# Optimization experiments

Hardware: AMD Instinct MI355X
Metric: run time of the kernel (lower is better)

## Reference

```python
import jax, jax.numpy as jnp
import numpy as np

PC_RANGE = (-50.0, -50.0, -4.0, 50.0, 50.0, 4.0)
IMG_H, IMG_W = 256.0, 704.0
EPS = 1e-5


def _bilinear_sample(feat, u, v):
    # feat [H,W,C]; u,v [M] in [0,1]; matches F.grid_sample(align_corners=False, padding_mode='zeros')
    H, W, _ = feat.shape
    x = u * W - 0.5
    y = v * H - 0.5
    x0 = jnp.floor(x)
    y0 = jnp.floor(y)
    dx = (x - x0)[:, None]
    dy = (y - y0)[:, None]
    x0 = x0.astype(jnp.int32)
    y0 = y0.astype(jnp.int32)

    def g(xi, yi):
        inb = ((xi >= 0) & (xi < W) & (yi >= 0) & (yi < H)).astype(feat.dtype)[:, None]
        return feat[jnp.clip(yi, 0, H - 1), jnp.clip(xi, 0, W - 1)] * inb

    return (g(x0, y0) * (1 - dx) * (1 - dy) + g(x0 + 1, y0) * dx * (1 - dy)
            + g(x0, y0 + 1) * (1 - dx) * dy + g(x0 + 1, y0 + 1) * dx * dy)


def _conv1x1(t, w, b):
    return jnp.einsum('bchw,oc->bohw', t, w) + b[None, :, None, None]


def _inorm(t, eps=1e-5):
    # InstanceNorm2d (affine=False): normalize per (b, c) over spatial dims
    m = t.mean(axis=(2, 3), keepdims=True)
    var = t.var(axis=(2, 3), keepdims=True)
    return (t - m) * jax.lax.rsqrt(var + eps)


def _forward(feat, lidar2img, bev_pos, pe_w1, pe_b1, pe_w2, pe_b2, pe_w3, pe_b3,
             c1_w, c1_b, c2_w, c2_b, c3_w, c3_b):
    B, N, C, Hf, Wf = feat.shape
    _, P, Hb, Wb, _ = bev_pos.shape
    Q = Hb * Wb
    lo = jnp.asarray(PC_RANGE[:3], feat.dtype)
    hi = jnp.asarray(PC_RANGE[3:], feat.dtype)
    # 'b p h w d -> b (h w) p d', then scale normalized coords into pc_range
    ref01 = jnp.transpose(bev_pos, (0, 2, 3, 1, 4)).reshape(B, Q, P, 3)
    ref = ref01 * (hi - lo) + lo
    # project through per-camera lidar2img (homogeneous)
    pts = jnp.concatenate([ref, jnp.ones_like(ref[..., :1])], axis=-1)  # [B,Q,P,4]
    cam = jnp.einsum('bnij,bqpj->bnqpi', lidar2img, pts)                # [B,N,Q,P,4]
    homo = cam[..., 2]
    z = jnp.maximum(homo, EPS)
    u = cam[..., 0] / z / IMG_W
    v = cam[..., 1] / z / IMG_H
    valid = ((homo > EPS) & (u > 0.0) & (u < 1.0) & (v > 0.0) & (v < 1.0)).astype(feat.dtype)
    # bilinear gather per camera; feats to channel-last ('b n (g c) h w -> (b g) n h w c', G=1)
    fmap = jnp.transpose(feat, (0, 1, 3, 4, 2)).reshape(B * N, Hf, Wf, C)
    samp = jax.vmap(_bilinear_sample)(fmap, u.reshape(B * N, Q * P), v.reshape(B * N, Q * P))
    samp = samp.reshape(B, N, Q, P, C) * valid[..., None]
    samp = samp.sum(axis=1)  # sum over cameras -> [B,Q,P,C]
    # PositionalEncodingMap(3 -> 256 -> 256 -> 128) on normalized reference points
    pe = jax.nn.relu(ref01 @ pe_w1 + pe_b1)
    pe = jax.nn.relu(pe @ pe_w2 + pe_b2)
    pe = pe @ pe_w3 + pe_b3
    samp = samp + pe
    # 'b (h w) g p c -> b (p g c) h w' with g=1
    x = jnp.transpose(samp.reshape(B, Hb, Wb, P, C), (0, 3, 4, 1, 2)).reshape(B, P * C, Hb, Wb)
    gelu = lambda t: jax.nn.gelu(t, approximate=False)
    x = gelu(_inorm(_conv1x1(x, c1_w, c1_b)))
    x = gelu(_inorm(_conv1x1(x, c2_w, c2_b)))
    x = _conv1x1(x, c3_w, c3_b)
    return x


def setup_inputs() -> dict:
    key = jax.random.key(0)
    ks = jax.random.split(key, 16)
    B, N, C, Hf, Wf = 1, 6, 128, 32, 88
    P, Hb, Wb = 4, 160, 160
    E = 128
    MID = 256
    s = 0.02
    return {
        'feat': jax.random.normal(ks[0], (B, N, C, Hf, Wf), jnp.float32),
        'lidar2img': jax.random.normal(ks[1], (B, N, 4, 4), jnp.float32),
        'bev_pos': jax.random.uniform(ks[2], (B, P, Hb, Wb, 3), jnp.float32),
        'pe_w1': jax.random.normal(ks[3], (3, MID), jnp.float32) * s,
        'pe_b1': jnp.zeros((MID,), jnp.float32),
        'pe_w2': jax.random.normal(ks[4], (MID, MID), jnp.float32) * s,
        'pe_b2': jnp.zeros((MID,), jnp.float32),
        'pe_w3': jax.random.normal(ks[5], (MID, E), jnp.float32) * s,
        'pe_b3': jnp.zeros((E,), jnp.float32),
        'c1_w': jax.random.normal(ks[6], (4 * E, P * 128), jnp.float32) * s,
        'c1_b': jnp.zeros((4 * E,), jnp.float32),
        'c2_w': jax.random.normal(ks[7], (E, 4 * E), jnp.float32) * s,
        'c2_b': jnp.zeros((E,), jnp.float32),
        'c3_w': jax.random.normal(ks[8], (E, E), jnp.float32) * s,
        'c3_b': jnp.zeros((E,), jnp.float32),
    }


def reference(feat, lidar2img, bev_pos, pe_w1, pe_b1, pe_w2, pe_b2, pe_w3, pe_b3,
              c1_w, c1_b, c2_w, c2_b, c3_w, c3_b):
    return _forward(feat, lidar2img, bev_pos, pe_w1, pe_b1, pe_w2, pe_b2, pe_w3, pe_b3,
                    c1_w, c1_b, c2_w, c2_b, c3_w, c3_b)
```

## Files before the change

kernel.cpp:

```cpp
#include <hip/hip_runtime.h>
#include <cstdint>
#include <cstddef>

using frag8 = __attribute__((ext_vector_type(8))) short;
using f32x4 = __attribute__((ext_vector_type(4))) float;

__device__ __forceinline__ float b2f_bits(unsigned short u) {
    union { uint32_t u32; float f; } x; x.u32 = ((uint32_t)u) << 16; return x.f;
}
__device__ __forceinline__ float b2f_lo(uint32_t pk) {
    return __builtin_bit_cast(float, pk << 16);
}
__device__ __forceinline__ float b2f_hi(uint32_t pk) {
    return __builtin_bit_cast(float, pk & 0xffff0000u);
}
__device__ __forceinline__ unsigned short f2b(float f) {
    uint32_t u = __builtin_bit_cast(uint32_t, f);
    uint32_t r = (u + 0x7fffu + ((u >> 16) & 1u)) >> 16;
    return (unsigned short)r;
}
__device__ __forceinline__ uint32_t cvtpk_bf16(float lo, float hi) {
    uint32_t r;
    asm("v_cvt_pk_bf16_f32 %0, %1, %2" : "=v"(r) : "v"(lo), "v"(hi));
    return r;
}

#define HF 32
#define WFEAT 88
#define NCAM 6
#define NPT 102400
#define BM 128
#define BN 128
#define BK 64

__global__ __launch_bounds__(256) void k_prep(const float* __restrict__ feat,
                                              const float* __restrict__ pw2,
                                              const float* __restrict__ pw3,
                                              const float* __restrict__ c1w,
                                              const float* __restrict__ c2w,
                                              const float* __restrict__ c3w,
                                              unsigned short* __restrict__ featT,
                                              unsigned short* __restrict__ W2Tb,
                                              unsigned short* __restrict__ W3Tb,
                                              unsigned short* __restrict__ C1Wb,
                                              unsigned short* __restrict__ C2Wb,
                                              unsigned short* __restrict__ C3Wb,
                                              float* __restrict__ stats) {
    __shared__ unsigned short tile[64 * 132];
    int b = blockIdx.x, t = threadIdx.x;
    if (b < 264) {
        int n = b / 44;
        int s0 = (b - n * 44) * 64;
        #pragma unroll
        for (int i = 0; i < 32; ++i) {
            int e = i * 256 + t;
            int c = e >> 6, sl = e & 63;
            tile[sl * 132 + c] = f2b(feat[(size_t)(n * 128 + c) * 2816 + s0 + sl]);
        }
        __syncthreads();
        #pragma unroll
        for (int j = 0; j < 8; ++j) {
            int flat = j * 1024 + t * 4;
            int sl = flat >> 7, c = flat & 127;
            ushort4 v = *(const ushort4*)(tile + sl * 132 + c);
            *(ushort4*)(featT + (size_t)(n * 2816 + s0 + sl) * 128 + c) = v;
        }
        return;
    }
    b -= 264;
    if (b < 256) {
        int idx = b * 256 + t;
        int r = idx >> 8, c = idx & 255;
        W2Tb[c * 256 + r] = f2b(pw2[idx]);
        return;
    }
    b -= 256;
    if (b < 128) {
        int idx = b * 256 + t;
        int r = idx >> 7, c = idx & 127;
        W3Tb[c * 256 + r] = f2b(pw3[idx]);
        return;
    }
    b -= 128;
    if (b < 1024) { int idx = b * 256 + t; C1Wb[idx] = f2b(c1w[idx]); return; }
    b -= 1024;
    if (b < 256)  { int idx = b * 256 + t; C2Wb[idx] = f2b(c2w[idx]); return; }
    b -= 256;
    if (b < 64)   { int idx = b * 256 + t; C3Wb[idx] = f2b(c3w[idx]); return; }
    #pragma unroll
    for (int j = 0; j < 10; ++j) stats[t * 10 + j] = 0.f;
}

__global__ __launch_bounds__(256) void k_sample2(const unsigned short* __restrict__ featT,
                                                 const float* __restrict__ l2i,
                                                 const float* __restrict__ bev,
                                                 unsigned short* __restrict__ samp) {
    int pt = blockIdx.x * 4 + (threadIdx.x >> 6);
    int lane = threadIdx.x & 63;
    int c2 = lane * 2;
    int q = pt >> 2, p = pt & 3;
    int h = q / 160, w = q - h * 160;
    const float* bv = bev + ((p * 160 + h) * 160 + w) * 3;
    float rx = bv[0] * 100.f - 50.f;
    float ry = bv[1] * 100.f - 50.f;
    float rz = bv[2] * 8.f - 4.f;
    float acc0 = 0.f, acc1 = 0.f;
    #pragma unroll
    for (int n = 0; n < NCAM; ++n) {
        const float* M = l2i + n * 16;
        float c0   = M[0] * rx + M[1] * ry + M[2]  * rz + M[3];
        float c1v  = M[4] * rx + M[5] * ry + M[6]  * rz + M[7];
        float homo = M[8] * rx + M[9] * ry + M[10] * rz + M[11];
        float z = fmaxf(homo, 1e-5f);
        float u = c0 / z / 704.0f;
        float v = c1v / z / 256.0f;
        if (homo > 1e-5f && u > 0.f && u < 1.f && v > 0.f && v < 1.f) {
            float fx = u * (float)WFEAT - 0.5f;
            float fy = v * (float)HF - 0.5f;
            float fx0 = floorf(fx), fy0 = floorf(fy);
            float dx = fx - fx0, dy = fy - fy0;
            int x0 = (int)fx0, y0 = (int)fy0;
            float wxa = (x0 < 0) ? dx : 1.f - dx;
            float wxb = (x0 >= 0 && x0 < WFEAT - 1) ? dx : 0.f;
            float wya = (y0 < 0) ? dy : 1.f - dy;
            float wyb = (y0 >= 0 && y0 < HF - 1) ? dy : 0.f;
            int bx = max(x0, 0), by = max(y0, 0);
            const unsigned short* base = featT + (((n * HF + by) * WFEAT + bx) << 7) + c2;
            uint32_t p00 = *(const uint32_t*)(base);
            uint32_t p01 = *(const uint32_t*)(base + 128);
            uint32_t p10 = *(const uint32_t*)(base + WFEAT * 128);
            uint32_t p11 = *(const uint32_t*)(base + WFEAT * 128 + 128);
            float w00 = wxa * wya, w01 = wxb * wya, w10 = wxa * wyb, w11 = wxb * wyb;
            acc0 += w00 * b2f_lo(p00) + w01 * b2f_lo(p01) + w10 * b2f_lo(p10) + w11 * b2f_lo(p11);
            acc1 += w00 * b2f_hi(p00) + w01 * b2f_hi(p01) + w10 * b2f_hi(p10) + w11 * b2f_hi(p11);
        }
    }
    uint32_t outpk = (uint32_t)f2b(acc0) | ((uint32_t)f2b(acc1) << 16);
    *(uint32_t*)(samp + (size_t)pt * 128 + c2) = outpk;
}

__device__ __forceinline__ void stage_tile(const unsigned short* __restrict__ g, int ld,
                                           unsigned short* lds, int wave, int lane) {
    #pragma unroll
    for (int j = 0; j < 4; ++j) {
        int idx = wave * 256 + j * 64 + lane;
        int r = idx >> 3;
        int cs = idx & 7;
        int cl = cs ^ (r & 7);
        __builtin_amdgcn_global_load_lds(
            (const __attribute__((address_space(1))) void*)(g + (size_t)r * ld + cl * 8),
            (__attribute__((address_space(3))) void*)(lds + wave * 2048 + j * 512),
            16, 0, 0);
    }
}

__device__ __forceinline__ frag8 frag_read(const unsigned short* lds, int row, int chunk) {
    return *(const frag8*)(lds + row * 64 + ((chunk ^ (row & 7)) << 3));
}

__device__ __forceinline__ void mma_tile(const unsigned short* As, const unsigned short* Bs,
                                         int wm, int wn, int lane, f32x4 (&acc)[4][4]) {
    int lm = lane & 15, lq = lane >> 4;
    #pragma unroll
    for (int kk = 0; kk < 2; ++kk) {
        frag8 a[4], b[4];
        #pragma unroll
        for (int t = 0; t < 4; ++t) a[t] = frag_read(As, wm * 64 + t * 16 + lm, kk * 4 + lq);
        #pragma unroll
        for (int t = 0; t < 4; ++t) b[t] = frag_read(Bs, wn * 64 + t * 16 + lm, kk * 4 + lq);
        #pragma unroll
        for (int tm = 0; tm < 4; ++tm)
            #pragma unroll
            for (int tn = 0; tn < 4; ++tn)
                acc[tm][tn] = __builtin_amdgcn_mfma_f32_16x16x32_bf16(a[tm], b[tn], acc[tm][tn], 0, 0, 0);
    }
}

template <int KT>
__device__ __forceinline__ void gemm_loop_pipe(const unsigned short* __restrict__ A, int ldA,
                                               const unsigned short* __restrict__ B, int ldB,
                                               unsigned short (*As)[BM * BK],
                                               unsigned short (*Bs)[BN * BK],
                                               int wave, int lane, int wm, int wn,
                                               f32x4 (&acc)[4][4]) {
    stage_tile(A, ldA, As[0], wave, lane);
    stage_tile(B, ldB, Bs[0], wave, lane);
    if (KT > 1) {
        stage_tile(A + BK, ldA, As[1], wave, lane);
        stage_tile(B + BK, ldB, Bs[1], wave, lane);
    }
    #pragma unroll
    for (int kt = 0; kt < KT; ++kt) {
        int cur = kt & 1;
        if (kt + 1 < KT) asm volatile("s_waitcnt vmcnt(8)" ::: "memory");
        else             asm volatile("s_waitcnt vmcnt(0)" ::: "memory");
        __builtin_amdgcn_s_barrier();
        mma_tile(As[cur], Bs[cur], wm, wn, lane, acc);
        asm volatile("s_waitcnt lgkmcnt(0)" ::: "memory");
        __builtin_amdgcn_s_barrier();
        if (kt + 2 < KT) {
            stage_tile(A + (kt + 2) * BK, ldA, As[cur], wave, lane);
            stage_tile(B + (kt + 2) * BK, ldB, Bs[cur], wave, lane);
        }
    }
}

__device__ __forceinline__ void build_h1_2(const float* __restrict__ wls, float x, float y, float z,
                                           int r, int c0, int kt, unsigned short* __restrict__ As) {
    #pragma unroll
    for (int j = 0; j < 2; ++j) {
        int cl = c0 + j;
        const float* wp = wls + kt * 64 + cl * 8;
        float4 a0l = *(const float4*)(wp),       a0h = *(const float4*)(wp + 4);
        float4 a1l = *(const float4*)(wp + 256), a1h = *(const float4*)(wp + 260);
        float4 a2l = *(const float4*)(wp + 512), a2h = *(const float4*)(wp + 516);
        float4 bbl = *(const float4*)(wp + 768), bbh = *(const float4*)(wp + 772);
        float v0 = fmaxf(x * a0l.x + y * a1l.x + z * a2l.x + bbl.x, 0.f);
        float v1 = fmaxf(x * a0l.y + y * a1l.y + z * a2l.y + bbl.y, 0.f);
        float v2 = fmaxf(x * a0l.z + y * a1l.z + z * a2l.z + bbl.z, 0.f);
        float v3 = fmaxf(x * a0l.w + y * a1l.w + z * a2l.w + bbl.w, 0.f);
        float v4 = fmaxf(x * a0h.x + y * a1h.x + z * a2h.x + bbh.x, 0.f);
        float v5 = fmaxf(x * a0h.y + y * a1h.y + z * a2h.y + bbh.y, 0.f);
        float v6 = fmaxf(x * a0h.z + y * a1h.z + z * a2h.z + bbh.z, 0.f);
        float v7 = fmaxf(x * a0h.w + y * a1h.w + z * a2h.w + bbh.w, 0.f);
        uint32_t q0 = cvtpk_bf16(v0, v1), q1 = cvtpk_bf16(v2, v3);
        uint32_t q2 = cvtpk_bf16(v4, v5), q3 = cvtpk_bf16(v6, v7);
        *(uint4*)(As + r * 64 + ((cl ^ (r & 7)) << 3)) = make_uint4(q0, q1, q2, q3);
    }
}

__global__ __launch_bounds__(256) void k_pe123(const float* __restrict__ bev,
                                               const float* __restrict__ pw1,
                                               const float* __restrict__ pb1,
                                               const unsigned short* __restrict__ W2t,
                                               const float* __restrict__ pb2,
                                               const unsigned short* __restrict__ W3t,
                                               const float* __restrict__ pb3,
                                               const unsigned short* __restrict__ samp,
                                               unsigned short* __restrict__ X) {
    __shared__ __align__(16) char smem[78592];
    unsigned short* As  = (unsigned short*)smem;
    unsigned short* Bs0 = (unsigned short*)(smem + 8192);
    unsigned short* Bs1 = (unsigned short*)(smem + 40960);
    float* wls  = (float*)(smem + 73728);
    float* bevs = (float*)(smem + 77824);
    int t = threadIdx.x, lane = t & 63, wave = t >> 6;
    int m0 = blockIdx.x * 64;
    {
        int i = t * 4;
        int j = i >> 8, c = i & 255;
        float4 v = (j < 3) ? *(const float4*)(pw1 + j * 256 + c)
                           : *(const float4*)(pb1 + c);
        *(float4*)(wls + i) = v;
    }
    if (t < 64) {
        int m = m0 + t;
        int q = m >> 2, p = m & 3;
        int h = q / 160, w = q - h * 160;
        const float* bv = bev + ((size_t)((p * 160 + h) * 160 + w)) * 3;
        bevs[t] = bv[0]; bevs[64 + t] = bv[1]; bevs[128 + t] = bv[2];
    }
    __syncthreads();
    int r = t & 63;
    int c0 = (t >> 6) * 2;
    float x = bevs[r], y = bevs[64 + r], z = bevs[128 + r];
    int lm = lane & 15, lq = lane >> 4;
    f32x4 acc[4][4] = {};
    stage_tile(W2t, 256, Bs0, wave, lane);
    stage_tile(W2t + 128 * 256, 256, Bs0 + 8192, wave, lane);
    stage_tile(W2t + BK, 256, Bs1, wave, lane);
    stage_tile(W2t + 128 * 256 + BK, 256, Bs1 + 8192, wave, lane);
    #pragma unroll
    for (int kt = 0; kt < 4; ++kt) {
        unsigned short* Bcur = (kt & 1) ? Bs1 : Bs0;
        build_h1_2(wls, x, y, z, r, c0, kt, As);
        asm volatile("s_waitcnt lgkmcnt(0)" ::: "memory");
        if (kt + 1 < 4) asm volatile("s_waitcnt vmcnt(8)" ::: "memory");
        else            asm volatile("s_waitcnt vmcnt(0)" ::: "memory");
        __builtin_amdgcn_s_barrier();
        #pragma unroll
        for (int kk = 0; kk < 2; ++kk) {
            int ch = kk * 4 + lq;
            frag8 a[4], b[4];
            #pragma unroll
            for (int tt = 0; tt < 4; ++tt) a[tt] = frag_read(As, tt * 16 + lm, ch);
            #pragma unroll
            for (int tn = 0; tn < 4; ++tn) b[tn] = frag_read(Bcur, wave * 64 + tn * 16 + lm, ch);
            #pragma unroll
            for (int tm = 0; tm < 4; ++tm)
                #pragma unroll
                for (int tn = 0; tn < 4; ++tn)
                    acc[tm][tn] = __builtin_amdgcn_mfma_f32_16x16x32_bf16(a[tm], b[tn], acc[tm][tn], 0, 0, 0);
        }
        asm volatile("s_waitcnt lgkmcnt(0)" ::: "memory");
        __builtin_amdgcn_s_barrier();
        if (kt + 2 < 4) {
            stage_tile(W2t + (kt + 2) * BK, 256, Bcur, wave, lane);
            stage_tile(W2t + 128 * 256 + (kt + 2) * BK, 256, Bcur + 8192, wave, lane);
        }
    }
    frag8 bw[4][2][2];
    #pragma unroll
    for (int kt = 0; kt < 4; ++kt)
        #pragma unroll
        for (int kk = 0; kk < 2; ++kk)
            #pragma unroll
            for (int tn = 0; tn < 2; ++tn) {
                int n2 = wave * 32 + tn * 16 + lm;
                bw[kt][kk][tn] = *(const frag8*)(W3t + (size_t)n2 * 256 + kt * 64 + (kk * 4 + lq) * 8);
            }
    unsigned short* H2s = Bs0;
    #pragma unroll
    for (int tn = 0; tn < 4; ++tn) {
        int c = tn * 16 + lm;
        int nn = wave * 64 + c;
        float bn = pb2[nn];
        int chw = c >> 3, e = c & 7;
        #pragma unroll
        for (int tm = 0; tm < 4; ++tm)
            #pragma unroll
            for (int rr = 0; rr < 4; ++rr) {
                int row = tm * 16 + lq * 4 + rr;
                H2s[wave * 4096 + row * 64 + ((chw ^ (row & 7)) << 3) + e] =
                    f2b(fmaxf(acc[tm][tn][rr] + bn, 0.f));
            }
    }
    asm volatile("s_waitcnt lgkmcnt(0)" ::: "memory");
    __builtin_amdgcn_s_barrier();
    f32x4 acc2[4][2] = {};
    #pragma unroll
    for (int kt = 0; kt < 4; ++kt)
        #pragma unroll
        for (int kk = 0; kk < 2; ++kk) {
            int ch = kk * 4 + lq;
            frag8 a[4];
            #pragma unroll
            for (int tm = 0; tm < 4; ++tm) a[tm] = frag_read(H2s + kt * 4096, tm * 16 + lm, ch);
            #pragma unroll
            for (int tm = 0; tm < 4; ++tm)
                #pragma unroll
                for (int tn = 0; tn < 2; ++tn)
                    acc2[tm][tn] = __builtin_amdgcn_mfma_f32_16x16x32_bf16(a[tm], bw[kt][kk][tn], acc2[tm][tn], 0, 0, 0);
        }
    #pragma unroll
    for (int tn = 0; tn < 2; ++tn) {
        int n2 = wave * 32 + tn * 16 + lm;
        float bn = pb3[n2];
        #pragma unroll
        for (int tm = 0; tm < 4; ++tm) {
            int mb = m0 + tm * 16 + lq * 4;
            #pragma unroll
            for (int rr = 0; rr < 4; ++rr) {
                size_t off = (size_t)(mb + rr) * 128 + n2;
                X[off] = f2b(acc2[tm][tn][rr] + bn + b2f_bits(samp[off]));
            }
        }
    }
}

template <int K, bool STATS>
__global__ __launch_bounds__(256) void k_gemm_conv(const unsigned short* __restrict__ A,
                                                   const unsigned short* __restrict__ Bt,
                                                   const float* __restrict__ bias,
                                                   unsigned short* __restrict__ Y, int ldY,
                                                   float* __restrict__ st, int C) {
    __shared__ unsigned short As[2][BM * BK], Bs[2][BN * BK];
    int lane = threadIdx.x & 63, wave = threadIdx.x >> 6;
    int wm = wave >> 1, wn = wave & 1;
    int m0 = blockIdx.x * BM, n0 = blockIdx.y * BN;
    f32x4 acc[4][4] = {};
    gemm_loop_pipe<K / BK>(A + (size_t)m0 * K, K, Bt + (size_t)n0 * K, K,
                           As, Bs, wave, lane, wm, wn, acc);
    int lm = lane & 15, lq = lane >> 4;
    #pragma unroll
    for (int tn = 0; tn < 4; ++tn) {
        int n = n0 + wn * 64 + tn * 16 + lm;
        float bn = bias[n];
        float s1 = 0.f, s2 = 0.f;
        #pragma unroll
        for (int tm = 0; tm < 4; ++tm) {
            int mb = m0 + wm * 64 + tm * 16 + lq * 4;
            #pragma unroll
            for (int rr = 0; rr < 4; ++rr) {
                float v = acc[tm][tn][rr] + bn;
                Y[(size_t)(mb + rr) * ldY + n] = f2b(v);
                if (STATS) { s1 += v; s2 += v * v; }
            }
        }
        if (STATS) {
            s1 += __shfl_xor(s1, 16); s1 += __shfl_xor(s1, 32);
            s2 += __shfl_xor(s2, 16); s2 += __shfl_xor(s2, 32);
            if (lq == 0) { atomicAdd(&st[n], s1); atomicAdd(&st[C + n], s2); }
        }
    }
}

__global__ __launch_bounds__(256) void k_gemm_conv3(const unsigned short* __restrict__ A,
                                                    const unsigned short* __restrict__ Bt,
                                                    const float* __restrict__ bias,
                                                    float* __restrict__ out) {
    __shared__ unsigned short As[2][BM * BK], Bs[2][BN * BK];
    int lane = threadIdx.x & 63, wave = threadIdx.x >> 6;
    int wm = wave >> 1, wn = wave & 1;
    int m0 = blockIdx.x * BM;
    f32x4 acc[4][4] = {};
    gemm_loop_pipe<2>(A + (size_t)m0 * 128, 128, Bt, 128, As, Bs, wave, lane, wm, wn, acc);
    int lm = lane & 15, lq = lane >> 4;
    #pragma unroll
    for (int tn = 0; tn < 4; ++tn) {
        int n = wn * 64 + tn * 16 + lm;
        float bn = bias[n];
        #pragma unroll
        for (int tm = 0; tm < 4; ++tm) {
            int mb = m0 + wm * 64 + tm * 16 + lq * 4;
            float4 pk;
            pk.x = acc[tm][tn][0] + bn;
            pk.y = acc[tm][tn][1] + bn;
            pk.z = acc[tm][tn][2] + bn;
            pk.w = acc[tm][tn][3] + bn;
            *(float4*)(out + (size_t)n * 25600 + mb) = pk;
        }
    }
}

__global__ void k_normgelu8f(const unsigned short* __restrict__ Y, const float* __restrict__ st,
                             unsigned short* __restrict__ X2, int Cmask, int C, float inv_n,
                             int total8) {
    int i8 = blockIdx.x * 256 + threadIdx.x;
    if (i8 >= total8) return;
    int e0 = i8 * 8;
    int c = e0 & Cmask;
    uint4 y = *(const uint4*)(Y + e0);
    float4 s1a = *(const float4*)(st + c);
    float4 s1b = *(const float4*)(st + c + 4);
    float4 s2a = *(const float4*)(st + C + c);
    float4 s2b = *(const float4*)(st + C + c + 4);
    float mu[8] = { s1a.x * inv_n, s1a.y * inv_n, s1a.z * inv_n, s1a.w * inv_n,
                    s1b.x * inv_n, s1b.y * inv_n, s1b.z * inv_n, s1b.w * inv_n };
    float sq[8] = { s2a.x, s2a.y, s2a.z, s2a.w, s2b.x, s2b.y, s2b.z, s2b.w };
    float rs[8];
    #pragma unroll
    for (int j = 0; j < 8; ++j) rs[j] = rsqrtf(sq[j] * inv_n - mu[j] * mu[j] + 1e-5f);
    const float is2 = 0.70710678118654752f;
    unsigned int yw[4] = {y.x, y.y, y.z, y.w};
    unsigned int ow[4];
    #pragma unroll
    for (int j = 0; j < 4; ++j) {
        float v0 = (b2f_bits((unsigned short)(yw[j] & 0xffffu)) - mu[j * 2]) * rs[j * 2];
        float v1 = (b2f_bits((unsigned short)(yw[j] >> 16)) - mu[j * 2 + 1]) * rs[j * 2 + 1];
        float g0 = 0.5f * v0 * (1.f + erff(v0 * is2));
        float g1 = 0.5f * v1 * (1.f + erff(v1 * is2));
        ow[j] = (uint32_t)f2b(g0) | ((uint32_t)f2b(g1) << 16);
    }
    *(uint4*)(X2 + e0) = make_uint4(ow[0], ow[1], ow[2], ow[3]);
}

extern "C" void kernel_launch(void* const* d_in, const int* in_sizes, int n_in,
                              void* d_out, int out_size, void* d_ws, size_t ws_size,
                              hipStream_t stream) {
    (void)in_sizes; (void)n_in; (void)out_size; (void)ws_size;
    const float* feat = (const float*)d_in[0];
    const float* l2i  = (const float*)d_in[1];
    const float* bev  = (const float*)d_in[2];
    const float* pw1  = (const float*)d_in[3];
    const float* pb1  = (const float*)d_in[4];
    const float* pw2  = (const float*)d_in[5];
    const float* pb2  = (const float*)d_in[6];
    const float* pw3  = (const float*)d_in[7];
    const float* pb3  = (const float*)d_in[8];
    const float* c1w  = (const float*)d_in[9];
    const float* c1b  = (const float*)d_in[10];
    const float* c2w  = (const float*)d_in[11];
    const float* c2b  = (const float*)d_in[12];
    const float* c3w  = (const float*)d_in[13];
    const float* c3b  = (const float*)d_in[14];
    float* outp = (float*)d_out;
    char* ws = (char*)d_ws;

    unsigned short* featT = (unsigned short*)(ws + 0);
    unsigned short* W2Tb  = (unsigned short*)(ws + 4348416);
    unsigned short* W3Tb  = (unsigned short*)(ws + 4479488);
    unsigned short* C1Wb  = (unsigned short*)(ws + 4545024);
    unsigned short* C2Wb  = (unsigned short*)(ws + 5069312);
    unsigned short* C3Wb  = (unsigned short*)(ws + 5200384);
    float* stats          = (float*)(ws + 5233152);
    char* BUF1 = ws + 17535488;
    char* BUF2 = ws + 69964288;
    char* BUF3 = ws + 122393088;

    float* st512 = stats;
    float* st128 = stats + 2048;

    unsigned short* samp = (unsigned short*)BUF3;
    unsigned short* X    = (unsigned short*)BUF1;
    unsigned short* Y1   = (unsigned short*)BUF2;
    unsigned short* X2   = (unsigned short*)BUF3;
    unsigned short* Y2   = (unsigned short*)BUF1;
    unsigned short* X3   = (unsigned short*)(BUF1 + 6553600);

    k_prep<<<1993, 256, 0, stream>>>(feat, pw2, pw3, c1w, c2w, c3w,
                                     featT, W2Tb, W3Tb, C1Wb, C2Wb, C3Wb, stats);

    k_sample2<<<25600, 256, 0, stream>>>(featT, l2i, bev, samp);

    k_pe123<<<1600, 256, 0, stream>>>(bev, pw1, pb1, W2Tb, pb2, W3Tb, pb3, samp, X);

    k_gemm_conv<512, true><<<dim3(200, 4), 256, 0, stream>>>(X, C1Wb, c1b, Y1, 512, st512, 512);
    k_normgelu8f<<<6400, 256, 0, stream>>>(Y1, st512, X2, 511, 512, 1.f / 25600.f, 1638400);

    k_gemm_conv<512, true><<<dim3(200, 1), 256, 0, stream>>>(X2, C2Wb, c2b, Y2, 128, st128, 128);
    k_normgelu8f<<<1600, 256, 0, stream>>>(Y2, st128, X3, 127, 128, 1.f / 25600.f, 409600);

    k_gemm_conv3<<<200, 256, 0, stream>>>(X3, C3Wb, c3b, outp);
}
```

Before: 292.9 us.

## Precompute per-point camera projection offsets and bilinear weights in prep kernel

Moves the per-camera projection, validity test and bilinear weight computation out of the sampling kernel, where it was redundantly computed by all 64 lanes per point, into the prep kernel with one thread per (camera, point). The sampling kernel now loads a precomputed offset and a float4 of weights per camera and only does the gathers and FMAs. In exchange it adds roughly 12 MB of extra workspace traffic, writes in prep and reads in sample, plus 2400 more prep blocks.

```diff
diff --git a/kernel.cpp b/kernel.cpp
--- a/kernel.cpp
+++ b/kernel.cpp
@@ -39,74 +39,28 @@
                                               const float* __restrict__ c1w,
                                               const float* __restrict__ c2w,
                                               const float* __restrict__ c3w,
+                                              const float* __restrict__ l2i,
+                                              const float* __restrict__ bev,
                                               unsigned short* __restrict__ featT,
                                               unsigned short* __restrict__ W2Tb,
                                               unsigned short* __restrict__ W3Tb,
                                               unsigned short* __restrict__ C1Wb,
                                               unsigned short* __restrict__ C2Wb,
                                               unsigned short* __restrict__ C3Wb,
-                                              float* __restrict__ stats) {
+                                              float* __restrict__ stats,
+                                              int* __restrict__ poff,
+                                              float4* __restrict__ pwts) {
     __shared__ unsigned short tile[64 * 132];
     int b = blockIdx.x, t = threadIdx.x;
-    if (b < 264) {
-        int n = b / 44;
-        int s0 = (b - n * 44) * 64;
-        #pragma unroll
-        for (int i = 0; i < 32; ++i) {
-            int e = i * 256 + t;
-            int c = e >> 6, sl = e & 63;
-            tile[sl * 132 + c] = f2b(feat[(size_t)(n * 128 + c) * 2816 + s0 + sl]);
-        }
-        __syncthreads();
-        #pragma unroll
-        for (int j = 0; j < 8; ++j) {
-            int flat = j * 1024 + t * 4;
-            int sl = flat >> 7, c = flat & 127;
-            ushort4 v = *(const ushort4*)(tile + sl * 132 + c);
-            *(ushort4*)(featT + (size_t)(n * 2816 + s0 + sl) * 128 + c) = v;
-        }
-        return;
-    }
-    b -= 264;
-    if (b < 256) {
+    if (b < 2400) {
         int idx = b * 256 + t;
-        int r = idx >> 8, c = idx & 255;
-        W2Tb[c * 256 + r] = f2b(pw2[idx]);
-        return;
-    }
-    b -= 256;
-    if (b < 128) {
-        int idx = b * 256 + t;
-        int r = idx >> 7, c = idx & 127;
-        W3Tb[c * 256 + r] = f2b(pw3[idx]);
-        return;
-    }
-    b -= 128;
-    if (b < 1024) { int idx = b * 256 + t; C1Wb[idx] = f2b(c1w[idx]); return; }
-    b -= 1024;
-    if (b < 256)  { int idx = b * 256 + t; C2Wb[idx] = f2b(c2w[idx]); return; }
-    b -= 256;
-    if (b < 64)   { int idx = b * 256 + t; C3Wb[idx] = f2b(c3w[idx]); return; }
-    #pragma unroll
-    for (int j = 0; j < 10; ++j) stats[t * 10 + j] = 0.f;
-}
-
-__global__ __launch_bounds__(256) void k_sample2(const unsigned short* __restrict__ featT,
-                                                 const float* __restrict__ l2i,
-                                                 const float* __restrict__ bev,
-                                                 unsigned short* __restrict__ samp) {
-    int pt = blockIdx.x * 4 + (threadIdx.x >> 6);
-    int lane = threadIdx.x & 63;
-    int c2 = lane * 2;
-    int q = pt >> 2, p = pt & 3;
-    int h = q / 160, w = q - h * 160;
-    const float* bv = bev + ((p * 160 + h) * 160 + w) * 3;
-    float rx = bv[0] * 100.f - 50.f;
-    float ry = bv[1] * 100.f - 50.f;
-    float rz = bv[2] * 8.f - 4.f;
-    float acc0 = 0.f, acc1 = 0.f;
-    #pragma unroll
-    for (int n = 0; n < NCAM; ++n) {
+        int n = idx / NPT, pt = idx - n * NPT;
+        int q = pt >> 2, p = pt & 3;
+        int h = q / 160, w = q - h * 160;
+        const float* bv = bev + ((p * 160 + h) * 160 + w) * 3;
+        float rx = bv[0] * 100.f - 50.f;
+        float ry = bv[1] * 100.f - 50.f;
+        float rz = bv[2] * 8.f - 4.f;
         const float* M = l2i + n * 16;
         float c0   = M[0] * rx + M[1] * ry + M[2]  * rz + M[3];
         float c1v  = M[4] * rx + M[5] * ry + M[6]  * rz + M[7];
@@ -114,25 +68,93 @@
         float z = fmaxf(homo, 1e-5f);
         float u = c0 / z / 704.0f;
         float v = c1v / z / 256.0f;
-        if (homo > 1e-5f && u > 0.f && u < 1.f && v > 0.f && v < 1.f) {
-            float fx = u * (float)WFEAT - 0.5f;
-            float fy = v * (float)HF - 0.5f;
-            float fx0 = floorf(fx), fy0 = floorf(fy);
-            float dx = fx - fx0, dy = fy - fy0;
-            int x0 = (int)fx0, y0 = (int)fy0;
-            float wxa = (x0 < 0) ? dx : 1.f - dx;
-            float wxb = (x0 >= 0 && x0 < WFEAT - 1) ? dx : 0.f;
-            float wya = (y0 < 0) ? dy : 1.f - dy;
-            float wyb = (y0 >= 0 && y0 < HF - 1) ? dy : 0.f;
-            int bx = max(x0, 0), by = max(y0, 0);
-            const unsigned short* base = featT + (((n * HF + by) * WFEAT + bx) << 7) + c2;
+        if (!(homo > 1e-5f && u > 0.f && u < 1.f && v > 0.f && v < 1.f)) {
+            poff[idx] = -1;
+            return;
+        }
+        float fx = u * (float)WFEAT - 0.5f;
+        float fy = v * (float)HF - 0.5f;
+        float fx0 = floorf(fx), fy0 = floorf(fy);
+        float dx = fx - fx0, dy = fy - fy0;
+        int x0 = (int)fx0, y0 = (int)fy0;
+        float wxa = (x0 < 0) ? dx : 1.f - dx;
+        float wxb = (x0 >= 0 && x0 < WFEAT - 1) ? dx : 0.f;
+        float wya = (y0 < 0) ? dy : 1.f - dy;
+        float wyb = (y0 >= 0 && y0 < HF - 1) ? dy : 0.f;
+        int bx = max(x0, 0), by = max(y0, 0);
+        poff[idx] = ((n * HF + by) * WFEAT + bx) << 7;
+        pwts[idx] = make_float4(wxa * wya, wxb * wya, wxa * wyb, wxb * wyb);
+        return;
+    }
+    b -= 2400;
+    if (b < 264) {
+        int n = b / 44;
+        int s0 = (b - n * 44) * 64;
+        #pragma unroll
+        for (int i = 0; i < 32; ++i) {
+            int e = i * 256 + t;
+            int c = e >> 6, sl = e & 63;
+            tile[sl * 132 + c] = f2b(feat[(size_t)(n * 128 + c) * 2816 + s0 + sl]);
+        }
+        __syncthreads();
+        #pragma unroll
+        for (int j = 0; j < 8; ++j) {
+            int flat = j * 1024 + t * 4;
+            int sl = flat >> 7, c = flat & 127;
+            ushort4 v = *(const ushort4*)(tile + sl * 132 + c);
+            *(ushort4*)(featT + (size_t)(n * 2816 + s0 + sl) * 128 + c) = v;
+        }
+        return;
+    }
+    b -= 264;
+    if (b < 256) {
+        int idx = b * 256 + t;
+        int r = idx >> 8, c = idx & 255;
+        W2Tb[c * 256 + r] = f2b(pw2[idx]);
+        return;
+    }
+    b -= 256;
+    if (b < 128) {
+        int idx = b * 256 + t;
+        int r = idx >> 7, c = idx & 127;
+        W3Tb[c * 256 + r] = f2b(pw3[idx]);
+        return;
+    }
+    b -= 128;
+    if (b < 1024) { int idx = b * 256 + t; C1Wb[idx] = f2b(c1w[idx]); return; }
+    b -= 1024;
+    if (b < 256)  { int idx = b * 256 + t; C2Wb[idx] = f2b(c2w[idx]); return; }
+    b -= 256;
+    if (b < 64)   { int idx = b * 256 + t; C3Wb[idx] = f2b(c3w[idx]); return; }
+    #pragma unroll
+    for (int j = 0; j < 10; ++j) stats[t * 10 + j] = 0.f;
+}
+
+__global__ __launch_bounds__(256) void k_sample2(const unsigned short* __restrict__ featT,
+                                                 const int* __restrict__ poff,
+                                                 const float4* __restrict__ pwts,
+                                                 unsigned short* __restrict__ samp) {
+    int pt = blockIdx.x * 4 + (threadIdx.x >> 6);
+    int lane = threadIdx.x & 63;
+    int c2 = lane * 2;
+    int offs[NCAM];
+    float4 ww[NCAM];
+    #pragma unroll
+    for (int n = 0; n < NCAM; ++n) offs[n] = poff[n * NPT + pt];
+    #pragma unroll
+    for (int n = 0; n < NCAM; ++n) ww[n] = pwts[n * NPT + pt];
+    float acc0 = 0.f, acc1 = 0.f;
+    #pragma unroll
+    for (int n = 0; n < NCAM; ++n) {
+        if (offs[n] >= 0) {
+            const unsigned short* base = featT + offs[n] + c2;
             uint32_t p00 = *(const uint32_t*)(base);
             uint32_t p01 = *(const uint32_t*)(base + 128);
             uint32_t p10 = *(const uint32_t*)(base + WFEAT * 128);
             uint32_t p11 = *(const uint32_t*)(base + WFEAT * 128 + 128);
-            float w00 = wxa * wya, w01 = wxb * wya, w10 = wxa * wyb, w11 = wxb * wyb;
-            acc0 += w00 * b2f_lo(p00) + w01 * b2f_lo(p01) + w10 * b2f_lo(p10) + w11 * b2f_lo(p11);
-            acc1 += w00 * b2f_hi(p00) + w01 * b2f_hi(p01) + w10 * b2f_hi(p10) + w11 * b2f_hi(p11);
+            float4 w = ww[n];
+            acc0 += w.x * b2f_lo(p00) + w.y * b2f_lo(p01) + w.z * b2f_lo(p10) + w.w * b2f_lo(p11);
+            acc1 += w.x * b2f_hi(p00) + w.y * b2f_hi(p01) + w.z * b2f_hi(p10) + w.w * b2f_hi(p11);
         }
     }
     uint32_t outpk = (uint32_t)f2b(acc0) | ((uint32_t)f2b(acc1) << 16);
@@ -484,6 +506,8 @@
     unsigned short* C2Wb  = (unsigned short*)(ws + 5069312);
     unsigned short* C3Wb  = (unsigned short*)(ws + 5200384);
     float* stats          = (float*)(ws + 5233152);
+    int*    poff          = (int*)(ws + 5247488);
+    float4* pwts          = (float4*)(ws + 7705088);
     char* BUF1 = ws + 17535488;
     char* BUF2 = ws + 69964288;
     char* BUF3 = ws + 122393088;
@@ -498,10 +522,11 @@
     unsigned short* Y2   = (unsigned short*)BUF1;
     unsigned short* X3   = (unsigned short*)(BUF1 + 6553600);
 
-    k_prep<<<1993, 256, 0, stream>>>(feat, pw2, pw3, c1w, c2w, c3w,
-                                     featT, W2Tb, W3Tb, C1Wb, C2Wb, C3Wb, stats);
-
-    k_sample2<<<25600, 256, 0, stream>>>(featT, l2i, bev, samp);
+    k_prep<<<4393, 256, 0, stream>>>(feat, pw2, pw3, c1w, c2w, c3w, l2i, bev,
+                                     featT, W2Tb, W3Tb, C1Wb, C2Wb, C3Wb, stats,
+                                     poff, pwts);
+
+    k_sample2<<<25600, 256, 0, stream>>>(featT, poff, pwts, samp);
 
     k_pe123<<<1600, 256, 0, stream>>>(bev, pw1, pb1, W2Tb, pb2, W3Tb, pb3, samp, X);
 
```

Result: faster. 264.3 us (-9.8%).
